# Optimization experiments

Hardware: AMD Instinct MI355X
Metric: run time of the kernel (lower is better)

The kernel has to match this reference:

```python
import jax, jax.numpy as jnp
import numpy as np

D_MODEL = 512
N_HEADS = 8
D_HEAD = D_MODEL // N_HEADS
SCALE = D_HEAD ** -0.5


def _rel_shift(x):
    # x: (b, h, qlen, klen) -> Transformer-XL relative shift
    b, h, qlen, klen = x.shape
    x = jnp.pad(x, ((0, 0), (0, 0), (0, 0), (1, 0)))        # (b,h,q,k+1)
    x = x.reshape(b, h, klen + 1, qlen)
    x = x[:, :, 1:, :].reshape(b, h, qlen, klen)
    return x


def setup_inputs() -> dict:
    key = jax.random.key(0)
    ks = jax.random.split(key, 12)
    B, S = 2, 2048
    P = 2 * S - 1
    w = lambda k, shape: (jax.random.normal(k, shape, jnp.float32) * 0.02)
    return {
        "x": jax.random.normal(ks[0], (B, S, D_MODEL), jnp.float32),
        "pos_emb": jax.random.normal(ks[1], (P, D_MODEL), jnp.float32),
        "Wq": w(ks[2], (D_MODEL, D_MODEL)), "bq": jnp.zeros((D_MODEL,), jnp.float32),
        "Wk": w(ks[3], (D_MODEL, D_MODEL)), "bk": jnp.zeros((D_MODEL,), jnp.float32),
        "Wv": w(ks[4], (D_MODEL, D_MODEL)), "bv": jnp.zeros((D_MODEL,), jnp.float32),
        "Wp": w(ks[5], (D_MODEL, D_MODEL)),
        "Wo": w(ks[6], (D_MODEL, D_MODEL)), "bo": jnp.zeros((D_MODEL,), jnp.float32),
        "pos_bias_u": w(ks[7], (N_HEADS, D_HEAD)),
        "pos_bias_v": w(ks[8], (N_HEADS, D_HEAD)),
    }


def reference(x, pos_emb, Wq, bq, Wk, bk, Wv, bv, Wp, Wo, bo, pos_bias_u, pos_bias_v):
    B, S, _ = x.shape
    # projections (torch Linear: y = x @ W^T + b; here W stored as (in, out))
    q = (x @ Wq + bq).reshape(B, S, N_HEADS, D_HEAD)
    k = (x @ Wk + bk).reshape(B, S, N_HEADS, D_HEAD)
    v = (x @ Wv + bv).reshape(B, S, N_HEADS, D_HEAD)
    p = (pos_emb @ Wp).reshape(-1, N_HEADS, D_HEAD)  # (2S-1, H, D)

    # content score: (q + u) @ k^T  -> (B,H,S,S)
    content = jnp.einsum("bshd,bthd->bhst", q + pos_bias_u, k)
    # position score: (q + v_bias) @ p^T -> (B,H,S,2S-1), then rel_shift
    pos = jnp.einsum("bshd,phd->bhsp", q + pos_bias_v, p)
    pos = _rel_shift(pos)[..., :S]  # trim to kv_len

    attn = jax.nn.softmax((content + pos) * SCALE, axis=-1)
    out = jnp.einsum("bhst,bthd->bshd", attn, v).reshape(B, S, D_MODEL)
    out = out @ Wo + bo
    return out
```

## Files before the change

### kernel.cpp

```cpp
#include <hip/hip_runtime.h>

#define DM    512
#define NH    8
#define DH    64
#define SEQ   2048
#define PLEN  4095
#define NB    2
#define ATT_SCALE 0.125f

typedef __attribute__((ext_vector_type(8))) _Float16 half8;
typedef __attribute__((ext_vector_type(4))) float   floatx4;

__global__ __launch_bounds__(256)
void prep(const float* __restrict__ x, const float* __restrict__ pe,
          const float* __restrict__ W0, const float* __restrict__ W1,
          const float* __restrict__ W2, const float* __restrict__ W3,
          const float* __restrict__ W4,
          _Float16* __restrict__ x16, _Float16* __restrict__ pe16,
          _Float16* __restrict__ Wt)
{
    __shared__ _Float16 tile[64 * 72];
    const int z = blockIdx.z;
    const int t = threadIdx.x;

    if (z < 2) {
        const float* src = z ? pe : x;
        _Float16* dst = z ? pe16 : x16;
        const long n = z ? (long)PLEN * DM : (long)NB * SEQ * DM;
        const long i = ((long)blockIdx.x * 256 + t) * 8;
        if (i >= n) return;
        float4 f0 = *(const float4*)(src + i);
        float4 f1 = *(const float4*)(src + i + 4);
        half8 o;
        o[0] = (_Float16)f0.x; o[1] = (_Float16)f0.y;
        o[2] = (_Float16)f0.z; o[3] = (_Float16)f0.w;
        o[4] = (_Float16)f1.x; o[5] = (_Float16)f1.y;
        o[6] = (_Float16)f1.z; o[7] = (_Float16)f1.w;
        *(half8*)(dst + i) = o;
        return;
    }
    if (blockIdx.x >= 64) return;
    const int wz = z - 2;
    const float* W = (wz == 0) ? W0 : (wz == 1) ? W1 : (wz == 2) ? W2
                   : (wz == 3) ? W3 : W4;
    _Float16* dst_base = Wt + (size_t)wz * DM * DM;
    const int n0 = (blockIdx.x & 7) * 64, k0 = (blockIdx.x >> 3) * 64;
    {
        const int kr = t >> 2, nch = (t & 3) * 16;
        const float* src = W + (size_t)(k0 + kr) * DM + n0 + nch;
        float4 f0 = *(const float4*)(src + 0);
        float4 f1 = *(const float4*)(src + 4);
        float4 f2 = *(const float4*)(src + 8);
        float4 f3 = *(const float4*)(src + 12);
        _Float16* trow = &tile[kr * 72 + nch];
        trow[0]  = (_Float16)f0.x; trow[1]  = (_Float16)f0.y;
        trow[2]  = (_Float16)f0.z; trow[3]  = (_Float16)f0.w;
        trow[4]  = (_Float16)f1.x; trow[5]  = (_Float16)f1.y;
        trow[6]  = (_Float16)f1.z; trow[7]  = (_Float16)f1.w;
        trow[8]  = (_Float16)f2.x; trow[9]  = (_Float16)f2.y;
        trow[10] = (_Float16)f2.z; trow[11] = (_Float16)f2.w;
        trow[12] = (_Float16)f3.x; trow[13] = (_Float16)f3.y;
        trow[14] = (_Float16)f3.z; trow[15] = (_Float16)f3.w;
    }
    __syncthreads();
    {
        const int nr = t >> 2, kch = (t & 3) * 16;
        half8 o0, o1;
#pragma unroll
        for (int i = 0; i < 8; ++i) o0[i] = tile[(kch + i) * 72 + nr];
#pragma unroll
        for (int i = 0; i < 8; ++i) o1[i] = tile[(kch + 8 + i) * 72 + nr];
        _Float16* dst = dst_base + (size_t)(n0 + nr) * DM + k0 + kch;
        *(half8*)dst = o0;
        *(half8*)(dst + 8) = o1;
    }
}

__global__ __launch_bounds__(256)
void gemm_qkvp(const _Float16* __restrict__ X, const _Float16* __restrict__ Pe,
               const _Float16* __restrict__ Wt,
               const float* __restrict__ bq, const float* __restrict__ bk,
               const float* __restrict__ bv, const float* __restrict__ bu,
               const float* __restrict__ bvb,
               _Float16* __restrict__ qu16, _Float16* __restrict__ qv16,
               _Float16* __restrict__ k16, _Float16* __restrict__ vt16,
               _Float16* __restrict__ p16)
{
    __shared__ _Float16 aS[64 * 72];
    __shared__ _Float16 wS[64 * 72];

    const int t = threadIdx.x;
    const int w = t >> 6, lane = t & 63, quad = lane >> 4, l16 = lane & 15;
    const int z = blockIdx.z;
    const int n0 = blockIdx.x * 64;
    const int m0 = blockIdx.y * 64;
    const int srow = t >> 2, sch = (t & 3) * 16;
    const _Float16* A = (z == 3) ? Pe : X;
    const _Float16* Wz = Wt + (size_t)z * DM * DM;

    int arow = m0 + srow;
    if (z == 3 && arow > PLEN - 1) arow = PLEN - 1;
    const _Float16* arowp = A + (size_t)arow * DM + sch;
    const _Float16* wrowp = Wz + (size_t)(n0 + srow) * DM + sch;

    floatx4 acc[4];
#pragma unroll
    for (int ct = 0; ct < 4; ++ct) acc[ct] = (floatx4){0.f, 0.f, 0.f, 0.f};

    half8 pa0 = *(const half8*)arowp;
    half8 pa1 = *(const half8*)(arowp + 8);
    half8 pw0 = *(const half8*)wrowp;
    half8 pw1 = *(const half8*)(wrowp + 8);

    for (int k0 = 0; k0 < DM; k0 += 64) {
        __syncthreads();
        *(half8*)&aS[srow * 72 + sch]     = pa0;
        *(half8*)&aS[srow * 72 + sch + 8] = pa1;
        *(half8*)&wS[srow * 72 + sch]     = pw0;
        *(half8*)&wS[srow * 72 + sch + 8] = pw1;
        __syncthreads();
        if (k0 + 64 < DM) {
            pa0 = *(const half8*)(arowp + k0 + 64);
            pa1 = *(const half8*)(arowp + k0 + 72);
            pw0 = *(const half8*)(wrowp + k0 + 64);
            pw1 = *(const half8*)(wrowp + k0 + 72);
        }
#pragma unroll
        for (int kb = 0; kb < 2; ++kb) {
            half8 af = *(const half8*)&aS[(16 * w + l16) * 72 + kb * 32 + quad * 8];
#pragma unroll
            for (int ct = 0; ct < 4; ++ct) {
                half8 bf = *(const half8*)&wS[(16 * ct + l16) * 72 + kb * 32 + quad * 8];
                acc[ct] = __builtin_amdgcn_mfma_f32_16x16x32_f16(af, bf, acc[ct], 0, 0, 0);
            }
        }
    }

    const int h = n0 >> 6;
    if (z == 0) {
#pragma unroll
        for (int ct = 0; ct < 4; ++ct) {
            const int n = n0 + 16 * ct + l16;
            const float bval = bq[n], uval = bu[n], vval = bvb[n];
#pragma unroll
            for (int r = 0; r < 4; ++r) {
                const int m = m0 + 16 * w + 4 * quad + r;
                const int b = m >> 11, s = m & 2047;
                const size_t dst = ((size_t)((h * NB + b) * SEQ) + s) * DH + (n & 63);
                const float q = acc[ct][r] + bval;
                qu16[dst] = (_Float16)((q + uval) * ATT_SCALE);
                qv16[dst] = (_Float16)((q + vval) * ATT_SCALE);
            }
        }
    } else if (z == 1) {
#pragma unroll
        for (int ct = 0; ct < 4; ++ct) {
            const int n = n0 + 16 * ct + l16;
            const float bval = bk[n];
#pragma unroll
            for (int r = 0; r < 4; ++r) {
                const int m = m0 + 16 * w + 4 * quad + r;
                const int b = m >> 11, s = m & 2047;
                k16[((size_t)((h * NB + b) * SEQ) + s) * DH + (n & 63)] =
                    (_Float16)(acc[ct][r] + bval);
            }
        }
    } else if (z == 2) {
        __syncthreads();
#pragma unroll
        for (int ct = 0; ct < 4; ++ct) {
            const float bval = bv[n0 + 16 * ct + l16];
#pragma unroll
            for (int r = 0; r < 4; ++r)
                aS[(16 * w + 4 * quad + r) * 72 + 16 * ct + l16] =
                    (_Float16)(acc[ct][r] + bval);
        }
        __syncthreads();
        const int b = m0 >> 11, s0 = m0 & 2047;
        const int drow = t >> 2;
        half8 o0, o1;
#pragma unroll
        for (int i = 0; i < 8; ++i) o0[i] = aS[(sch + i) * 72 + drow];
#pragma unroll
        for (int i = 0; i < 8; ++i) o1[i] = aS[(sch + 8 + i) * 72 + drow];
        _Float16* dst = vt16 + ((size_t)((h * NB + b) * DH) + drow) * SEQ + s0 + sch;
        *(half8*)dst = o0;
        *(half8*)(dst + 8) = o1;
    } else {
#pragma unroll
        for (int ct = 0; ct < 4; ++ct) {
            const int n = n0 + 16 * ct + l16;
#pragma unroll
            for (int r = 0; r < 4; ++r) {
                const int m = m0 + 16 * w + 4 * quad + r;
                if (m < PLEN)
                    p16[((size_t)h * PLEN + m) * DH + (n & 63)] = (_Float16)acc[ct][r];
            }
        }
    }
}

__global__ __launch_bounds__(256, 2)
void relattn_mfma(const _Float16* __restrict__ QU,
                  const _Float16* __restrict__ QV,
                  const _Float16* __restrict__ Kp,
                  const _Float16* __restrict__ VT,
                  const _Float16* __restrict__ Pp,
                  _Float16* __restrict__ Out)
{
    __shared__ _Float16 kS[64 * 72];
    __shared__ _Float16 pS[128 * 72];
    __shared__ _Float16 vS[64 * 72];
    __shared__ _Float16 tS[64 * 88];

    const int t = threadIdx.x;
    const int w = t >> 6, lane = t & 63, quad = lane >> 4, l16 = lane & 15;
    const int i0 = blockIdx.x * 64;
    const int h = blockIdx.y, b = blockIdx.z;
    const size_t hb = (size_t)(h * NB + b);
    const int cbase = 48 - 16 * w;

    half8 qa[2], va[2];
    {
        const _Float16* qrow = QU + (hb * SEQ + i0 + 16 * w + l16) * DH + quad * 8;
        const _Float16* vrow = QV + (hb * SEQ + i0 + 16 * w + l16) * DH + quad * 8;
        qa[0] = *(const half8*)qrow;       qa[1] = *(const half8*)(qrow + 32);
        va[0] = *(const half8*)vrow;       va[1] = *(const half8*)(vrow + 32);
    }

    floatx4 O[4];
    float lsum[4] = {0.f, 0.f, 0.f, 0.f};
#pragma unroll
    for (int ct = 0; ct < 4; ++ct) O[ct] = (floatx4){0.f, 0.f, 0.f, 0.f};

    const int srow = t >> 2, schunk = (t & 3) * 16;
    const int prow = t >> 1, pch = (t & 1) * 32;

    const _Float16* Kbase = Kp + hb * SEQ * DH;
    const _Float16* Vbase = VT + hb * DH * SEQ;
    const _Float16* Pbase = Pp + (size_t)h * PLEN * DH;
    const int rbase0 = (SEQ - 1) - i0 - 63;

    half8 pk0, pk1, pv0, pv1;
    half8 pp0 = {}, pp1 = {}, pp2 = {}, pp3 = {};
    {
        const _Float16* src = Kbase + (size_t)srow * DH + schunk;
        pk0 = *(const half8*)src;
        pk1 = *(const half8*)(src + 8);
        const _Float16* vsrc = Vbase + (size_t)srow * SEQ + schunk;
        pv0 = *(const half8*)vsrc;
        pv1 = *(const half8*)(vsrc + 8);
        if (prow < 127) {
            const _Float16* psrc = Pbase + (size_t)(rbase0 + prow) * DH + pch;
            pp0 = *(const half8*)(psrc + 0);
            pp1 = *(const half8*)(psrc + 8);
            pp2 = *(const half8*)(psrc + 16);
            pp3 = *(const half8*)(psrc + 24);
        }
    }

    for (int j0 = 0; j0 < SEQ; j0 += 64) {
        __syncthreads();

        *(half8*)&kS[srow * 72 + schunk]     = pk0;
        *(half8*)&kS[srow * 72 + schunk + 8] = pk1;
        *(half8*)&vS[srow * 72 + schunk]     = pv0;
        *(half8*)&vS[srow * 72 + schunk + 8] = pv1;
        if (prow < 127) {
            *(half8*)&pS[prow * 72 + pch + 0]  = pp0;
            *(half8*)&pS[prow * 72 + pch + 8]  = pp1;
            *(half8*)&pS[prow * 72 + pch + 16] = pp2;
            *(half8*)&pS[prow * 72 + pch + 24] = pp3;
        }
        __syncthreads();

        if (j0 + 64 < SEQ) {
            const _Float16* src = Kbase + (size_t)(j0 + 64 + srow) * DH + schunk;
            pk0 = *(const half8*)src;
            pk1 = *(const half8*)(src + 8);
            const _Float16* vsrc = Vbase + (size_t)srow * SEQ + j0 + 64 + schunk;
            pv0 = *(const half8*)vsrc;
            pv1 = *(const half8*)(vsrc + 8);
            if (prow < 127) {
                const _Float16* psrc = Pbase + (size_t)(rbase0 + j0 + 64 + prow) * DH + pch;
                pp0 = *(const half8*)(psrc + 0);
                pp1 = *(const half8*)(psrc + 8);
                pp2 = *(const half8*)(psrc + 16);
                pp3 = *(const half8*)(psrc + 24);
            }
        }

        {
            floatx4 Tacc[5];
#pragma unroll
            for (int c2 = 0; c2 < 5; ++c2) Tacc[c2] = (floatx4){0.f, 0.f, 0.f, 0.f};
#pragma unroll
            for (int kb = 0; kb < 2; ++kb) {
#pragma unroll
                for (int c2 = 0; c2 < 5; ++c2) {
                    half8 bf = *(const half8*)&pS[(cbase + 16 * c2 + l16) * 72 + kb * 32 + quad * 8];
                    Tacc[c2] = __builtin_amdgcn_mfma_f32_16x16x32_f16(va[kb], bf, Tacc[c2], 0, 0, 0);
                }
            }
#pragma unroll
            for (int c2 = 0; c2 < 5; ++c2)
#pragma unroll
                for (int r = 0; r < 4; ++r)
                    tS[(16 * w + 4 * quad + r) * 88 + 16 * c2 + l16] = (_Float16)Tacc[c2][r];
        }
        asm volatile("" ::: "memory");

        floatx4 Sc[4];
#pragma unroll
        for (int ct = 0; ct < 4; ++ct) Sc[ct] = (floatx4){0.f, 0.f, 0.f, 0.f};
#pragma unroll
        for (int kb = 0; kb < 2; ++kb) {
#pragma unroll
            for (int ct = 0; ct < 4; ++ct) {
                half8 bf = *(const half8*)&kS[(16 * ct + l16) * 72 + kb * 32 + quad * 8];
                Sc[ct] = __builtin_amdgcn_mfma_f32_16x16x32_f16(qa[kb], bf, Sc[ct], 0, 0, 0);
            }
        }
#pragma unroll
        for (int ct = 0; ct < 4; ++ct)
#pragma unroll
            for (int r = 0; r < 4; ++r) {
                const int il16 = 4 * quad + r;
                const int c = 16 * ct + l16 - il16 + 15;
                const float e = __expf(Sc[ct][r] +
                                       (float)tS[(16 * w + il16) * 88 + c]);
                Sc[ct][r] = e;
                lsum[r] += e;
            }
        asm volatile("" ::: "memory");

#pragma unroll
        for (int ct = 0; ct < 4; ++ct)
#pragma unroll
            for (int r = 0; r < 4; ++r)
                tS[(16 * w + 4 * quad + r) * 88 + 16 * ct + l16] = (_Float16)Sc[ct][r];
        asm volatile("" ::: "memory");

#pragma unroll
        for (int kb = 0; kb < 2; ++kb) {
            half8 af = *(const half8*)&tS[(16 * w + l16) * 88 + kb * 32 + quad * 8];
#pragma unroll
            for (int ct = 0; ct < 4; ++ct) {
                half8 bf = *(const half8*)&vS[(16 * ct + l16) * 72 + kb * 32 + quad * 8];
                O[ct] = __builtin_amdgcn_mfma_f32_16x16x32_f16(af, bf, O[ct], 0, 0, 0);
            }
        }
        asm volatile("" ::: "memory");
    }

#pragma unroll
    for (int r = 0; r < 4; ++r) {
#pragma unroll
        for (int m = 1; m < 16; m <<= 1) lsum[r] += __shfl_xor(lsum[r], m);
        const float inv = 1.f / lsum[r];
        _Float16* orow = Out + (size_t)(b * SEQ + i0 + 16 * w + 4 * quad + r) * DM + h * DH;
#pragma unroll
        for (int ct = 0; ct < 4; ++ct)
            orow[16 * ct + l16] = (_Float16)(O[ct][r] * inv);
    }
}

__global__ __launch_bounds__(256)
void gemm_out(const _Float16* __restrict__ A, const _Float16* __restrict__ Wt,
              const float* __restrict__ bias, float* __restrict__ Out)
{
    __shared__ _Float16 aS[64 * 72];
    __shared__ _Float16 wS[64 * 72];

    const int t = threadIdx.x;
    const int w = t >> 6, lane = t & 63, quad = lane >> 4, l16 = lane & 15;
    const int n0 = blockIdx.x * 64;
    const int m0 = blockIdx.y * 64;
    const int srow = t >> 2, sch = (t & 3) * 16;

    const _Float16* arowp = A + (size_t)(m0 + srow) * DM + sch;
    const _Float16* wrowp = Wt + (size_t)(n0 + srow) * DM + sch;

    floatx4 acc[4];
#pragma unroll
    for (int ct = 0; ct < 4; ++ct) acc[ct] = (floatx4){0.f, 0.f, 0.f, 0.f};

    half8 pa0 = *(const half8*)arowp;
    half8 pa1 = *(const half8*)(arowp + 8);
    half8 pw0 = *(const half8*)wrowp;
    half8 pw1 = *(const half8*)(wrowp + 8);

    for (int k0 = 0; k0 < DM; k0 += 64) {
        __syncthreads();
        *(half8*)&aS[srow * 72 + sch]     = pa0;
        *(half8*)&aS[srow * 72 + sch + 8] = pa1;
        *(half8*)&wS[srow * 72 + sch]     = pw0;
        *(half8*)&wS[srow * 72 + sch + 8] = pw1;
        __syncthreads();
        if (k0 + 64 < DM) {
            pa0 = *(const half8*)(arowp + k0 + 64);
            pa1 = *(const half8*)(arowp + k0 + 72);
            pw0 = *(const half8*)(wrowp + k0 + 64);
            pw1 = *(const half8*)(wrowp + k0 + 72);
        }
#pragma unroll
        for (int kb = 0; kb < 2; ++kb) {
            half8 af = *(const half8*)&aS[(16 * w + l16) * 72 + kb * 32 + quad * 8];
#pragma unroll
            for (int ct = 0; ct < 4; ++ct) {
                half8 bf = *(const half8*)&wS[(16 * ct + l16) * 72 + kb * 32 + quad * 8];
                acc[ct] = __builtin_amdgcn_mfma_f32_16x16x32_f16(af, bf, acc[ct], 0, 0, 0);
            }
        }
    }

#pragma unroll
    for (int ct = 0; ct < 4; ++ct) {
        const int n = n0 + 16 * ct + l16;
        const float bval = bias[n];
#pragma unroll
        for (int r = 0; r < 4; ++r) {
            const int m = m0 + 16 * w + 4 * quad + r;
            Out[(size_t)m * DM + n] = acc[ct][r] + bval;
        }
    }
}

extern "C" void kernel_launch(void* const* d_in, const int* in_sizes, int n_in,
                              void* d_out, int out_size, void* d_ws, size_t ws_size,
                              hipStream_t stream)
{
    (void)in_sizes; (void)n_in; (void)out_size; (void)ws_size;
    const float* x   = (const float*)d_in[0];
    const float* pe  = (const float*)d_in[1];
    const float* Wq  = (const float*)d_in[2];
    const float* bq  = (const float*)d_in[3];
    const float* Wk  = (const float*)d_in[4];
    const float* bk  = (const float*)d_in[5];
    const float* Wv  = (const float*)d_in[6];
    const float* bv  = (const float*)d_in[7];
    const float* Wp  = (const float*)d_in[8];
    const float* Wo  = (const float*)d_in[9];
    const float* bo  = (const float*)d_in[10];
    const float* pbu = (const float*)d_in[11];
    const float* pbv = (const float*)d_in[12];
    float* out = (float*)d_out;

    const size_t nX  = (size_t)NB * SEQ * DM;
    const size_t nPe = (size_t)PLEN * DM;
    const size_t nW  = (size_t)DM * DM;
    const size_t nH  = (size_t)NH * NB * SEQ * DH;
    const size_t nPh = (size_t)NH * PLEN * DH;

    _Float16* x16  = (_Float16*)d_ws;
    _Float16* pe16 = x16 + nX;
    _Float16* wt   = pe16 + nPe;
    _Float16* qu16 = wt + 5 * nW;
    _Float16* qv16 = qu16 + nH;
    _Float16* k16  = qv16 + nH;
    _Float16* vt16 = k16 + nH;
    _Float16* p16  = vt16 + nH;
    _Float16* ow16 = p16 + nPh;

    dim3 blk(256);
    prep<<<dim3(1024, 1, 7), blk, 0, stream>>>(x, pe, Wq, Wk, Wv, Wp, Wo,
                                               x16, pe16, wt);
    gemm_qkvp<<<dim3(8, 64, 4), blk, 0, stream>>>(x16, pe16, wt,
                                                  bq, bk, bv, pbu, pbv,
                                                  qu16, qv16, k16, vt16, p16);
    relattn_mfma<<<dim3(SEQ / 64, NH, NB), blk, 0, stream>>>(
        qu16, qv16, k16, vt16, p16, ow16);
    gemm_out<<<dim3(8, 64), blk, 0, stream>>>(ow16, wt + 4 * nW, bo, out);
}
```

Baseline: 187.3 us.

## Split attention key range across two blocks and combine partial results

Splits each attention block's key loop into two halves handled by separate blocks, writing unnormalized fp32 partial outputs and row sums. A new combine kernel adds the partials and normalizes. The tS scratch now aliases pS with an extra barrier, and launch bounds are raised for higher occupancy. This trades extra global traffic and a kernel launch for more parallelism and latency hiding.

```diff
diff --git a/kernel.cpp b/kernel.cpp
--- a/kernel.cpp
+++ b/kernel.cpp
@@ -200,25 +200,28 @@
     }
 }
 
-__global__ __launch_bounds__(256, 2)
+__global__ __launch_bounds__(256, 4)
 void relattn_mfma(const _Float16* __restrict__ QU,
                   const _Float16* __restrict__ QV,
                   const _Float16* __restrict__ Kp,
                   const _Float16* __restrict__ VT,
                   const _Float16* __restrict__ Pp,
-                  _Float16* __restrict__ Out)
+                  float* __restrict__ Opart,
+                  float* __restrict__ Lpart)
 {
     __shared__ _Float16 kS[64 * 72];
     __shared__ _Float16 pS[128 * 72];
     __shared__ _Float16 vS[64 * 72];
-    __shared__ _Float16 tS[64 * 88];
+    _Float16* const tS = pS;
 
     const int t = threadIdx.x;
     const int w = t >> 6, lane = t & 63, quad = lane >> 4, l16 = lane & 15;
     const int i0 = blockIdx.x * 64;
-    const int h = blockIdx.y, b = blockIdx.z;
+    const int h = blockIdx.y;
+    const int b = blockIdx.z & 1, jh = blockIdx.z >> 1;
     const size_t hb = (size_t)(h * NB + b);
     const int cbase = 48 - 16 * w;
+    const int jbeg = jh * (SEQ / 2), jend = jbeg + (SEQ / 2);
 
     half8 qa[2], va[2];
     {
@@ -244,14 +247,14 @@
     half8 pk0, pk1, pv0, pv1;
     half8 pp0 = {}, pp1 = {}, pp2 = {}, pp3 = {};
     {
-        const _Float16* src = Kbase + (size_t)srow * DH + schunk;
+        const _Float16* src = Kbase + (size_t)(jbeg + srow) * DH + schunk;
         pk0 = *(const half8*)src;
         pk1 = *(const half8*)(src + 8);
-        const _Float16* vsrc = Vbase + (size_t)srow * SEQ + schunk;
+        const _Float16* vsrc = Vbase + (size_t)srow * SEQ + jbeg + schunk;
         pv0 = *(const half8*)vsrc;
         pv1 = *(const half8*)(vsrc + 8);
         if (prow < 127) {
-            const _Float16* psrc = Pbase + (size_t)(rbase0 + prow) * DH + pch;
+            const _Float16* psrc = Pbase + (size_t)(rbase0 + jbeg + prow) * DH + pch;
             pp0 = *(const half8*)(psrc + 0);
             pp1 = *(const half8*)(psrc + 8);
             pp2 = *(const half8*)(psrc + 16);
@@ -259,7 +262,7 @@
         }
     }
 
-    for (int j0 = 0; j0 < SEQ; j0 += 64) {
+    for (int j0 = jbeg; j0 < jend; j0 += 64) {
         __syncthreads();
 
         *(half8*)&kS[srow * 72 + schunk]     = pk0;
@@ -274,7 +277,7 @@
         }
         __syncthreads();
 
-        if (j0 + 64 < SEQ) {
+        if (j0 + 64 < jend) {
             const _Float16* src = Kbase + (size_t)(j0 + 64 + srow) * DH + schunk;
             pk0 = *(const half8*)src;
             pk1 = *(const half8*)(src + 8);
@@ -290,24 +293,23 @@
             }
         }
 
-        {
-            floatx4 Tacc[5];
-#pragma unroll
-            for (int c2 = 0; c2 < 5; ++c2) Tacc[c2] = (floatx4){0.f, 0.f, 0.f, 0.f};
-#pragma unroll
-            for (int kb = 0; kb < 2; ++kb) {
-#pragma unroll
-                for (int c2 = 0; c2 < 5; ++c2) {
-                    half8 bf = *(const half8*)&pS[(cbase + 16 * c2 + l16) * 72 + kb * 32 + quad * 8];
-                    Tacc[c2] = __builtin_amdgcn_mfma_f32_16x16x32_f16(va[kb], bf, Tacc[c2], 0, 0, 0);
-                }
-            }
-#pragma unroll
-            for (int c2 = 0; c2 < 5; ++c2)
-#pragma unroll
-                for (int r = 0; r < 4; ++r)
-                    tS[(16 * w + 4 * quad + r) * 88 + 16 * c2 + l16] = (_Float16)Tacc[c2][r];
-        }
+        floatx4 Tacc[5];
+#pragma unroll
+        for (int c2 = 0; c2 < 5; ++c2) Tacc[c2] = (floatx4){0.f, 0.f, 0.f, 0.f};
+#pragma unroll
+        for (int kb = 0; kb < 2; ++kb) {
+#pragma unroll
+            for (int c2 = 0; c2 < 5; ++c2) {
+                half8 bf = *(const half8*)&pS[(cbase + 16 * c2 + l16) * 72 + kb * 32 + quad * 8];
+                Tacc[c2] = __builtin_amdgcn_mfma_f32_16x16x32_f16(va[kb], bf, Tacc[c2], 0, 0, 0);
+            }
+        }
+        __syncthreads();
+#pragma unroll
+        for (int c2 = 0; c2 < 5; ++c2)
+#pragma unroll
+            for (int r = 0; r < 4; ++r)
+                tS[(16 * w + 4 * quad + r) * 88 + 16 * c2 + l16] = (_Float16)Tacc[c2][r];
         asm volatile("" ::: "memory");
 
         floatx4 Sc[4];
@@ -353,16 +355,47 @@
         asm volatile("" ::: "memory");
     }
 
+    float* Op = Opart + (size_t)jh * NB * SEQ * DM;
+    float* Lp = Lpart + (size_t)jh * NH * NB * SEQ;
 #pragma unroll
     for (int r = 0; r < 4; ++r) {
 #pragma unroll
         for (int m = 1; m < 16; m <<= 1) lsum[r] += __shfl_xor(lsum[r], m);
-        const float inv = 1.f / lsum[r];
-        _Float16* orow = Out + (size_t)(b * SEQ + i0 + 16 * w + 4 * quad + r) * DM + h * DH;
+        const int row = i0 + 16 * w + 4 * quad + r;
+        if (l16 == 0) Lp[hb * SEQ + row] = lsum[r];
+        float* orow = Op + (size_t)(b * SEQ + row) * DM + h * DH;
 #pragma unroll
         for (int ct = 0; ct < 4; ++ct)
-            orow[16 * ct + l16] = (_Float16)(O[ct][r] * inv);
-    }
+            orow[16 * ct + l16] = O[ct][r];
+    }
+}
+
+__global__ __launch_bounds__(256)
+void attn_combine(const float* __restrict__ O0, const float* __restrict__ O1,
+                  const float* __restrict__ L0, const float* __restrict__ L1,
+                  _Float16* __restrict__ Out)
+{
+    const int e = (blockIdx.x * 256 + threadIdx.x) * 8;
+    const int m = e >> 9;
+    const int col = e & 511;
+    const int h = col >> 6;
+    const int b = m >> 11, i = m & 2047;
+    const int li = (h * NB + b) * SEQ + i;
+    const float inv = 1.f / (L0[li] + L1[li]);
+    float4 a0 = *(const float4*)(O0 + e);
+    float4 a1 = *(const float4*)(O0 + e + 4);
+    float4 c0 = *(const float4*)(O1 + e);
+    float4 c1 = *(const float4*)(O1 + e + 4);
+    half8 o;
+    o[0] = (_Float16)((a0.x + c0.x) * inv);
+    o[1] = (_Float16)((a0.y + c0.y) * inv);
+    o[2] = (_Float16)((a0.z + c0.z) * inv);
+    o[3] = (_Float16)((a0.w + c0.w) * inv);
+    o[4] = (_Float16)((a1.x + c1.x) * inv);
+    o[5] = (_Float16)((a1.y + c1.y) * inv);
+    o[6] = (_Float16)((a1.z + c1.z) * inv);
+    o[7] = (_Float16)((a1.w + c1.w) * inv);
+    *(half8*)(Out + e) = o;
 }
 
 __global__ __launch_bounds__(256)
@@ -451,6 +484,7 @@
     const size_t nW  = (size_t)DM * DM;
     const size_t nH  = (size_t)NH * NB * SEQ * DH;
     const size_t nPh = (size_t)NH * PLEN * DH;
+    const size_t nL  = (size_t)NH * NB * SEQ;
 
     _Float16* x16  = (_Float16*)d_ws;
     _Float16* pe16 = x16 + nX;
@@ -461,6 +495,8 @@
     _Float16* vt16 = k16 + nH;
     _Float16* p16  = vt16 + nH;
     _Float16* ow16 = p16 + nPh;
+    float*    opart = (float*)(ow16 + nX);
+    float*    lpart = opart + 2 * nX;
 
     dim3 blk(256);
     prep<<<dim3(1024, 1, 7), blk, 0, stream>>>(x, pe, Wq, Wk, Wv, Wp, Wo,
@@ -468,7 +504,9 @@
     gemm_qkvp<<<dim3(8, 64, 4), blk, 0, stream>>>(x16, pe16, wt,
                                                   bq, bk, bv, pbu, pbv,
                                                   qu16, qv16, k16, vt16, p16);
-    relattn_mfma<<<dim3(SEQ / 64, NH, NB), blk, 0, stream>>>(
-        qu16, qv16, k16, vt16, p16, ow16);
+    relattn_mfma<<<dim3(SEQ / 64, NH, NB * 2), blk, 0, stream>>>(
+        qu16, qv16, k16, vt16, p16, opart, lpart);
+    attn_combine<<<dim3((unsigned)(nX / (256 * 8))), blk, 0, stream>>>(
+        opart, opart + nX, lpart, lpart + nL, ow16);
     gemm_out<<<dim3(8, 64), blk, 0, stream>>>(ow16, wt + 4 * nW, bo, out);
 }
```

After: 194.2 us. 3.6% more time.
